# Kernel tuning notes

Measured on AMD Instinct MI355X. Metric: run time of the kernel, lower is better.

## Reference

```python
import jax, jax.numpy as jnp
import numpy as np

EPS = 1e-6
GROUPS = 32


def setup_inputs() -> dict:
    key = jax.random.key(0)
    ks = jax.random.split(key, 6)
    B, C, T = 4, 256, 4096
    s = 1.0 / np.sqrt(C)
    return {
        "x": jax.random.normal(ks[0], (B, C, T), dtype=jnp.float32),
        "gn_scale": jnp.ones((C,), jnp.float32),
        "gn_bias": jnp.zeros((C,), jnp.float32),
        "wq": jax.random.normal(ks[1], (C, C), jnp.float32) * s,
        "bq": jnp.zeros((C,), jnp.float32),
        "wk": jax.random.normal(ks[2], (C, C), jnp.float32) * s,
        "bk": jnp.zeros((C,), jnp.float32),
        "wv": jax.random.normal(ks[3], (C, C), jnp.float32) * s,
        "bv": jnp.zeros((C,), jnp.float32),
        "wo": jax.random.normal(ks[4], (C, C), jnp.float32) * s,
        "bo": jnp.zeros((C,), jnp.float32),
    }


def _group_norm(x, scale, bias):
    B, C, T = x.shape
    h = x.reshape(B, GROUPS, C // GROUPS, T)
    mean = h.mean(axis=(2, 3), keepdims=True)
    var = ((h - mean) ** 2).mean(axis=(2, 3), keepdims=True)
    h = (h - mean) * jax.lax.rsqrt(var + EPS)
    h = h.reshape(B, C, T)
    return h * scale[None, :, None] + bias[None, :, None]


def _conv1x1(w, b, h):
    # Conv1d kernel_size=1 == per-timestep channel matmul
    return jnp.einsum('oc,bct->bot', w, h) + b[None, :, None]


def reference(x, gn_scale, gn_bias, wq, bq, wk, bk, wv, bv, wo, bo):
    B, C, T = x.shape
    h = _group_norm(x, gn_scale, gn_bias)
    q = _conv1x1(wq, bq, h)  # [B,C,T]
    k = _conv1x1(wk, bk, h)
    v = _conv1x1(wv, bv, h)
    # w_[b,q,k] = sum_c q[b,c,q] k[b,c,k] * C**-0.5, softmax over k
    w = jnp.einsum('bcq,bck->bqk', q, k) * (C ** -0.5)
    w = jax.nn.softmax(w, axis=2)
    # torch code: h_[b, i, c] = sum_j w[b, j, i] * v_perm[b, j, c]
    h = jnp.einsum('bqk,bcq->bck', w, v)  # [B,C,T]
    h = _conv1x1(wo, bo, h)
    return x + h
```

## Files before the change

### kernel.cpp

```cpp
#include <hip/hip_runtime.h>

typedef float f32x4 __attribute__((ext_vector_type(4)));
typedef short s16x8 __attribute__((ext_vector_type(8)));

#define MOFF 12.0f

__device__ __forceinline__ unsigned short f2bf(float f) {
  unsigned int u = __float_as_uint(f);
  u += 0x7fffu + ((u >> 16) & 1u);
  return (unsigned short)(u >> 16);
}

template <typename T>
__device__ __forceinline__ void gload16(const T* g, T* l) {
  __builtin_amdgcn_global_load_lds(
      (const __attribute__((address_space(1))) void*)g,
      (__attribute__((address_space(3))) void*)l, 16, 0, 0);
}

__global__ __launch_bounds__(256) void gn_stats_k(const float* __restrict__ x,
                                                  float* __restrict__ meanv,
                                                  float* __restrict__ rstdv) {
  const int bg = blockIdx.x;
  const float4* base = (const float4*)(x + (size_t)bg * 8 * 4096);
  float s = 0.f, q = 0.f;
  for (int i = threadIdx.x; i < 8192; i += 256) {
    float4 v = base[i];
    s += v.x + v.y + v.z + v.w;
    q += v.x * v.x + v.y * v.y + v.z * v.z + v.w * v.w;
  }
  for (int o = 32; o; o >>= 1) { s += __shfl_down(s, o); q += __shfl_down(q, o); }
  __shared__ float ss[4], sq[4];
  const int wv = threadIdx.x >> 6;
  if ((threadIdx.x & 63) == 0) { ss[wv] = s; sq[wv] = q; }
  __syncthreads();
  if (threadIdx.x == 0) {
    s = ss[0] + ss[1] + ss[2] + ss[3];
    q = sq[0] + sq[1] + sq[2] + sq[3];
    float mu = s * (1.f / 32768.f);
    float var = q * (1.f / 32768.f) - mu * mu;
    meanv[bg] = mu;
    rstdv[bg] = rsqrtf(var + 1e-6f);
  }
}

__global__ __launch_bounds__(256) void gn_apply_t_k(const float* __restrict__ x,
    const float* __restrict__ gamma, const float* __restrict__ beta,
    const float* __restrict__ meanv, const float* __restrict__ rstdv,
    unsigned short* __restrict__ hT) {
  __shared__ unsigned short tile[64][72];
  const int b = blockIdx.z, c0 = blockIdx.y * 64, t0 = blockIdx.x * 64;
  const int tid = threadIdx.x;
  {
    const int tr = tid >> 4, tc = (tid & 15) * 4;
    const float* xb = x + ((size_t)b * 256 + c0) * 4096 + t0;
    for (int p2 = 0; p2 < 4; ++p2) {
      int cl = p2 * 16 + tr;
      int c = c0 + cl;
      int bg = b * 32 + (c >> 3);
      float ga = gamma[c] * rstdv[bg];
      float be = beta[c] - meanv[bg] * ga;
      float4 v = *(const float4*)(xb + (size_t)cl * 4096 + tc);
      tile[cl][tc + 0] = f2bf(v.x * ga + be);
      tile[cl][tc + 1] = f2bf(v.y * ga + be);
      tile[cl][tc + 2] = f2bf(v.z * ga + be);
      tile[cl][tc + 3] = f2bf(v.w * ga + be);
    }
  }
  __syncthreads();
  {
    const int orow = tid >> 3, oc = (tid & 7) * 8;
    unsigned short* hb = hT + ((size_t)b * 4096 + t0) * 256 + c0;
    for (int p2 = 0; p2 < 2; ++p2) {
      int tl = p2 * 32 + orow;
      s16x8 w;
#pragma unroll
      for (int j = 0; j < 8; ++j) w[j] = (short)tile[oc + j][tl];
      *(s16x8*)(hb + (size_t)tl * 256 + oc) = w;
    }
  }
}

enum { EPI_WT = 0, EPI_PB = 1, EPI_FIN = 3 };

template <bool AF32, int EPI>
__global__ __launch_bounds__(256) void gemm64_k(
    const void* __restrict__ Ap, long long sA, int lda,
    const unsigned short* __restrict__ Bp, long long sB, int ldb,
    void* __restrict__ Op, long long sO, int ldo,
    const float* __restrict__ bias,
    const float* __restrict__ xadd, long long sX,
    float scale, int K) {
  __shared__ s16x8 lsA[4][64];
  __shared__ s16x8 lsB[4][64];
  const int tid = threadIdx.x;
  const int m0 = blockIdx.y * 64, n0 = blockIdx.x * 64;
  const int z = blockIdx.z;
  const int lane = tid & 63, wv = tid >> 6;
  const int lrow = lane & 15, lg = lane >> 4;
  const int srow = tid >> 2, scg = tid & 3;
  const int swrow = srow ^ (scg << 1);

  f32x4 acc[4];
#pragma unroll
  for (int i = 0; i < 4; ++i) acc[i] = (f32x4){0.f, 0.f, 0.f, 0.f};

  const unsigned short* Bb = Bp + (size_t)z * sB + (size_t)(n0 + srow) * ldb + scg * 8;

  for (int k0 = 0; k0 < K; k0 += 32) {
    if (AF32) {
      const float* ap = (const float*)Ap + (size_t)z * sA + (size_t)(m0 + srow) * lda + k0 + scg * 8;
      float4 v0 = *(const float4*)ap;
      float4 v1 = *(const float4*)(ap + 4);
      s16x8 w;
      w[0] = (short)f2bf(v0.x); w[1] = (short)f2bf(v0.y);
      w[2] = (short)f2bf(v0.z); w[3] = (short)f2bf(v0.w);
      w[4] = (short)f2bf(v1.x); w[5] = (short)f2bf(v1.y);
      w[6] = (short)f2bf(v1.z); w[7] = (short)f2bf(v1.w);
      lsA[scg][swrow] = w;
    } else {
      const unsigned short* ap = (const unsigned short*)Ap + (size_t)z * sA + (size_t)(m0 + srow) * lda + k0 + scg * 8;
      lsA[scg][swrow] = *(const s16x8*)ap;
    }
    lsB[scg][swrow] = *(const s16x8*)(Bb + k0);
    __syncthreads();
    s16x8 af = lsA[lg][(wv * 16 + lrow) ^ (lg << 1)];
#pragma unroll
    for (int nt = 0; nt < 4; ++nt) {
      s16x8 bf = lsB[lg][(nt * 16 + lrow) ^ (lg << 1)];
      acc[nt] = __builtin_amdgcn_mfma_f32_16x16x32_bf16(af, bf, acc[nt], 0, 0, 0);
    }
    __syncthreads();
  }

  const int mb = m0 + wv * 16 + lg * 4;
  float bv0 = 0.f, bv1 = 0.f, bv2 = 0.f, bv3 = 0.f;
  if (bias) { bv0 = bias[mb]; bv1 = bias[mb + 1]; bv2 = bias[mb + 2]; bv3 = bias[mb + 3]; }
#pragma unroll
  for (int nt = 0; nt < 4; ++nt) {
    const int n = n0 + nt * 16 + lrow;
    if (EPI == EPI_WT) {
      ushort4 pk;
      pk.x = f2bf((acc[nt][0] + bv0) * scale);
      pk.y = f2bf((acc[nt][1] + bv1) * scale);
      pk.z = f2bf((acc[nt][2] + bv2) * scale);
      pk.w = f2bf((acc[nt][3] + bv3) * scale);
      *(ushort4*)((unsigned short*)Op + (size_t)z * sO + (size_t)n * ldo + mb) = pk;
    } else if (EPI == EPI_PB) {
      unsigned short* o = (unsigned short*)Op + (size_t)z * sO;
      o[(size_t)(mb + 0) * ldo + n] = f2bf(acc[nt][0] + bv0);
      o[(size_t)(mb + 1) * ldo + n] = f2bf(acc[nt][1] + bv1);
      o[(size_t)(mb + 2) * ldo + n] = f2bf(acc[nt][2] + bv2);
      o[(size_t)(mb + 3) * ldo + n] = f2bf(acc[nt][3] + bv3);
    } else {
      float* o = (float*)Op + (size_t)z * sO;
      const float* xa = xadd + (size_t)z * sX;
      o[(size_t)(mb + 0) * ldo + n] = acc[nt][0] + bv0 + xa[(size_t)(mb + 0) * ldo + n];
      o[(size_t)(mb + 1) * ldo + n] = acc[nt][1] + bv1 + xa[(size_t)(mb + 1) * ldo + n];
      o[(size_t)(mb + 2) * ldo + n] = acc[nt][2] + bv2 + xa[(size_t)(mb + 2) * ldo + n];
      o[(size_t)(mb + 3) * ldo + n] = acc[nt][3] + bv3 + xa[(size_t)(mb + 3) * ldo + n];
    }
  }
}

__global__ __launch_bounds__(256) void attn_stats3_k(
    const unsigned short* __restrict__ qT,
    const unsigned short* __restrict__ kT,
    float* __restrict__ pl) {
  __shared__ unsigned short kbuf[2][64 * 256];
  const int tid = threadIdx.x;
  const int b = blockIdx.z;
  const int Q0 = blockIdx.x * 256;
  const int kc = blockIdx.y;
  const int lane = tid & 63, wq = tid >> 6;
  const int lrow = lane & 15, lg = lane >> 4;

  const unsigned short* qb = qT + (size_t)b * (4096 * 256);
  const unsigned short* kb = kT + (size_t)b * (4096 * 256);

  s16x8 af[4][8];
#pragma unroll
  for (int mt = 0; mt < 4; ++mt)
#pragma unroll
    for (int ks = 0; ks < 8; ++ks)
      af[mt][ks] = *(const s16x8*)(qb + (size_t)(Q0 + wq * 64 + mt * 16 + lrow) * 256 + ks * 32 + lg * 8);

  float sl[4][4];
#pragma unroll
  for (int mt = 0; mt < 4; ++mt)
#pragma unroll
    for (int j = 0; j < 4; ++j) sl[mt][j] = 0.f;

  int cur = 0;
  {
    const unsigned short* src = kb + (size_t)(kc * 512) * 256;
#pragma unroll
    for (int rep = 0; rep < 8; ++rep) {
      int i = rep * 256 + tid;
      int row = i >> 5, c8 = i & 31;
      gload16(src + (size_t)row * 256 + (c8 ^ (row & 7)) * 8, &kbuf[0][(i - lane) * 8]);
    }
  }
  __syncthreads();

  for (int it = 0; it < 8; ++it) {
    if (it + 1 < 8) {
      const unsigned short* src = kb + (size_t)(kc * 512 + (it + 1) * 64) * 256;
#pragma unroll
      for (int rep = 0; rep < 8; ++rep) {
        int i = rep * 256 + tid;
        int row = i >> 5, c8 = i & 31;
        gload16(src + (size_t)row * 256 + (c8 ^ (row & 7)) * 8, &kbuf[cur ^ 1][(i - lane) * 8]);
      }
    }
#pragma unroll
    for (int nt = 0; nt < 4; ++nt) {
      f32x4 acc[4];
#pragma unroll
      for (int mt = 0; mt < 4; ++mt) acc[mt] = (f32x4){0.f, 0.f, 0.f, 0.f};
#pragma unroll
      for (int ks = 0; ks < 8; ++ks) {
        int row = nt * 16 + lrow;
        int ch = (ks * 4 + lg) ^ (row & 7);
        s16x8 bf = *(const s16x8*)&kbuf[cur][row * 256 + ch * 8];
#pragma unroll
        for (int mt = 0; mt < 4; ++mt)
          acc[mt] = __builtin_amdgcn_mfma_f32_16x16x32_bf16(af[mt][ks], bf, acc[mt], 0, 0, 0);
      }
#pragma unroll
      for (int mt = 0; mt < 4; ++mt)
#pragma unroll
        for (int j = 0; j < 4; ++j) sl[mt][j] += __expf(acc[mt][j] - MOFF);
    }
    __syncthreads();
    cur ^= 1;
  }
#pragma unroll
  for (int mt = 0; mt < 4; ++mt)
#pragma unroll
    for (int j = 0; j < 4; ++j) {
      float v = sl[mt][j];
      v += __shfl_xor(v, 1);
      v += __shfl_xor(v, 2);
      v += __shfl_xor(v, 4);
      v += __shfl_xor(v, 8);
      sl[mt][j] = v;
    }
  if (lrow == 0) {
    float* plb = pl + ((size_t)kc * 4 + b) * 4096;
#pragma unroll
    for (int mt = 0; mt < 4; ++mt)
#pragma unroll
      for (int j = 0; j < 4; ++j)
        plb[Q0 + wq * 64 + mt * 16 + lg * 4 + j] = sl[mt][j];
  }
}

__global__ __launch_bounds__(256) void make_r_k(const float* __restrict__ pl,
                                                float* __restrict__ ra) {
  int i = blockIdx.x * 256 + threadIdx.x;
  int b = i >> 12, q = i & 4095;
  float l = 0.f;
#pragma unroll
  for (int kc = 0; kc < 8; ++kc) l += pl[((size_t)kc * 4 + b) * 4096 + q];
  ra[i] = 1.f / l;
}

__global__ __launch_bounds__(512) void attn_pv5_k(
    const unsigned short* __restrict__ qT,
    const unsigned short* __restrict__ kT,
    const unsigned short* __restrict__ vb,
    const float* __restrict__ ra,
    unsigned short* __restrict__ aT) {
  __shared__ unsigned short qbuf[2][128 * 256];
  __shared__ unsigned short P[64 * 128];
  const int tid = threadIdx.x;
  const int pidx = blockIdx.x;
  const int z = (pidx >> 1) & 3;
  const int kt = ((pidx >> 3) << 1) | (pidx & 1);
  const int K0 = kt * 64;
  const int lane = tid & 63, w = tid >> 6;
  const int lrow = lane & 15, lg = lane >> 4;
  const int khw = w >> 2;
  const int qqw = w & 3;

  const unsigned short* qg = qT + (size_t)z * (4096 * 256);
  const unsigned short* kg = kT + (size_t)z * (4096 * 256);
  const unsigned short* vg = vb + (size_t)z * (4096 * 256);
  const float* rg = ra + (size_t)z * 4096;

  s16x8 kf[2][8];
#pragma unroll
  for (int ktl = 0; ktl < 2; ++ktl)
#pragma unroll
    for (int ks = 0; ks < 8; ++ks)
      kf[ktl][ks] = *(const s16x8*)(kg + (size_t)(K0 + khw * 32 + ktl * 16 + lrow) * 256 + ks * 32 + lg * 8);

  f32x4 oacc[2][4];
#pragma unroll
  for (int ct = 0; ct < 2; ++ct)
#pragma unroll
    for (int nt = 0; nt < 4; ++nt) oacc[ct][nt] = (f32x4){0.f, 0.f, 0.f, 0.f};

  int cur = 0;
  {
#pragma unroll
    for (int rep = 0; rep < 8; ++rep) {
      int i = rep * 512 + tid;
      int row = i >> 5, c8 = i & 31;
      gload16(qg + (size_t)row * 256 + (c8 ^ (row & 7)) * 8, &qbuf[0][(i - lane) * 8]);
    }
  }
  __syncthreads();

  for (int qi = 0; qi < 32; ++qi) {
    const int q0 = qi * 128;
    s16x8 vf[2][4];
#pragma unroll
    for (int ct = 0; ct < 2; ++ct)
#pragma unroll
      for (int qs = 0; qs < 4; ++qs)
        vf[ct][qs] = *(const s16x8*)(vg + (size_t)(w * 32 + ct * 16 + lrow) * 4096 + q0 + qs * 32 + lg * 8);
    if (qi + 1 < 32) {
      const unsigned short* src = qg + (size_t)(q0 + 128) * 256;
#pragma unroll
      for (int rep = 0; rep < 8; ++rep) {
        int i = rep * 512 + tid;
        int row = i >> 5, c8 = i & 31;
        gload16(src + (size_t)row * 256 + (c8 ^ (row & 7)) * 8, &qbuf[cur ^ 1][(i - lane) * 8]);
      }
    }
    f32x4 sacc[2][2];
#pragma unroll
    for (int ktl = 0; ktl < 2; ++ktl)
#pragma unroll
      for (int qt = 0; qt < 2; ++qt) sacc[ktl][qt] = (f32x4){0.f, 0.f, 0.f, 0.f};
#pragma unroll
    for (int qt = 0; qt < 2; ++qt) {
#pragma unroll
      for (int ks = 0; ks < 8; ++ks) {
        int row = qqw * 32 + qt * 16 + lrow;
        int ch = (ks * 4 + lg) ^ (row & 7);
        s16x8 qf = *(const s16x8*)&qbuf[cur][row * 256 + ch * 8];
        sacc[0][qt] = __builtin_amdgcn_mfma_f32_16x16x32_bf16(kf[0][ks], qf, sacc[0][qt], 0, 0, 0);
        sacc[1][qt] = __builtin_amdgcn_mfma_f32_16x16x32_bf16(kf[1][ks], qf, sacc[1][qt], 0, 0, 0);
      }
    }
#pragma unroll
    for (int qt = 0; qt < 2; ++qt) {
      const int ql = qqw * 32 + qt * 16 + lrow;
      const float rv = rg[q0 + ql];
#pragma unroll
      for (int ktl = 0; ktl < 2; ++ktl)
#pragma unroll
        for (int j = 0; j < 4; ++j) {
          int k = khw * 32 + ktl * 16 + lg * 4 + j;
          float p = __expf(sacc[ktl][qt][j] - MOFF) * rv;
          P[k * 128 + (((ql >> 3) ^ (k & 7)) << 3) + (ql & 7)] = f2bf(p);
        }
    }
    __syncthreads();
#pragma unroll
    for (int qs = 0; qs < 4; ++qs) {
      s16x8 pf[4];
#pragma unroll
      for (int nt = 0; nt < 4; ++nt) {
        int k = nt * 16 + lrow;
        pf[nt] = *(const s16x8*)&P[k * 128 + (((qs * 4 + lg) ^ (k & 7)) << 3)];
      }
#pragma unroll
      for (int ct = 0; ct < 2; ++ct)
#pragma unroll
        for (int nt = 0; nt < 4; ++nt)
          oacc[ct][nt] = __builtin_amdgcn_mfma_f32_16x16x32_bf16(vf[ct][qs], pf[nt], oacc[ct][nt], 0, 0, 0);
    }
    __syncthreads();
    cur ^= 1;
  }
  unsigned short* ab = aT + (size_t)z * (4096 * 256);
#pragma unroll
  for (int ct = 0; ct < 2; ++ct)
#pragma unroll
    for (int nt = 0; nt < 4; ++nt) {
      int k = K0 + nt * 16 + lrow;
      int c = w * 32 + ct * 16 + lg * 4;
      ushort4 pk;
      pk.x = f2bf(oacc[ct][nt][0]);
      pk.y = f2bf(oacc[ct][nt][1]);
      pk.z = f2bf(oacc[ct][nt][2]);
      pk.w = f2bf(oacc[ct][nt][3]);
      *(ushort4*)(ab + (size_t)k * 256 + c) = pk;
    }
}

extern "C" void kernel_launch(void* const* d_in, const int* in_sizes, int n_in,
                              void* d_out, int out_size, void* d_ws, size_t ws_size,
                              hipStream_t stream) {
  const float* x   = (const float*)d_in[0];
  const float* gns = (const float*)d_in[1];
  const float* gnb = (const float*)d_in[2];
  const float* wq  = (const float*)d_in[3];
  const float* bq  = (const float*)d_in[4];
  const float* wk  = (const float*)d_in[5];
  const float* bk  = (const float*)d_in[6];
  const float* wvp = (const float*)d_in[7];
  const float* bv  = (const float*)d_in[8];
  const float* wo  = (const float*)d_in[9];
  const float* bo  = (const float*)d_in[10];
  float* out = (float*)d_out;

  const int B = 4, C = 256, T = 4096;
  const long long TCe = (long long)T * C;

  char* p = (char*)d_ws;
  unsigned short* hT = (unsigned short*)p; p += (size_t)B * TCe * 2;
  unsigned short* qT = (unsigned short*)p; p += (size_t)B * TCe * 2;
  unsigned short* kT = (unsigned short*)p; p += (size_t)B * TCe * 2;
  unsigned short* vb = (unsigned short*)p; p += (size_t)B * TCe * 2;
  unsigned short* aT = (unsigned short*)p; p += (size_t)B * TCe * 2;
  float* gmean = (float*)p; p += 512;
  float* grstd = (float*)p; p += 512;
  float* pl = (float*)p; p += (size_t)8 * B * T * 4;
  float* ra = (float*)p; p += (size_t)B * T * 4;

  gn_stats_k<<<B * 32, 256, 0, stream>>>(x, gmean, grstd);
  gn_apply_t_k<<<dim3(T / 64, C / 64, B), 256, 0, stream>>>(x, gns, gnb, gmean, grstd, hT);

  gemm64_k<true, EPI_WT><<<dim3(T / 64, C / 64, B), 256, 0, stream>>>(
      wq, 0, C, hT, TCe, C, qT, TCe, C, bq, nullptr, 0, 0.0625f, C);
  gemm64_k<true, EPI_WT><<<dim3(T / 64, C / 64, B), 256, 0, stream>>>(
      wk, 0, C, hT, TCe, C, kT, TCe, C, bk, nullptr, 0, 1.0f, C);
  gemm64_k<true, EPI_PB><<<dim3(T / 64, C / 64, B), 256, 0, stream>>>(
      wvp, 0, C, hT, TCe, C, vb, TCe, T, bv, nullptr, 0, 1.0f, C);

  attn_stats3_k<<<dim3(T / 256, 8, B), 256, 0, stream>>>(qT, kT, pl);
  make_r_k<<<B * T / 256, 256, 0, stream>>>(pl, ra);
  attn_pv5_k<<<256, 512, 0, stream>>>(qT, kT, vb, ra, aT);

  gemm64_k<true, EPI_FIN><<<dim3(T / 64, C / 64, B), 256, 0, stream>>>(
      wo, 0, C, aT, TCe, C, out, TCe, T, bo, x, TCe, 1.0f, C);
}
```

Measured before the change: 206.9 us.

## Split PV attention over query ranges, fold softmax reciprocal into V projection

Reworks the attention PV kernel so each block handles a 128-key tile and one quarter of the queries, with 256-thread blocks, per-wave private P tiles and a smaller Q double buffer. The per-query softmax normalization (1/l) is moved into the V-projection epilogue, which removes the per-element multiply in the hot loop. Partial outputs go to a large fp32 workspace and a new merge kernel sums the four query splits and converts to bf16. The intent is more parallelism and occupancy with less block-level sync, at the cost of extra memory traffic for the fp32 partials and one more launch.

```diff
diff --git a/kernel.cpp b/kernel.cpp
--- a/kernel.cpp
+++ b/kernel.cpp
@@ -81,7 +81,7 @@
   }
 }
 
-enum { EPI_WT = 0, EPI_PB = 1, EPI_FIN = 3 };
+enum { EPI_WT = 0, EPI_PB = 1, EPI_FIN = 3, EPI_PBR = 4 };
 
 template <bool AF32, int EPI>
 __global__ __launch_bounds__(256) void gemm64_k(
@@ -152,6 +152,13 @@
       o[(size_t)(mb + 1) * ldo + n] = f2bf(acc[nt][1] + bv1);
       o[(size_t)(mb + 2) * ldo + n] = f2bf(acc[nt][2] + bv2);
       o[(size_t)(mb + 3) * ldo + n] = f2bf(acc[nt][3] + bv3);
+    } else if (EPI == EPI_PBR) {
+      unsigned short* o = (unsigned short*)Op + (size_t)z * sO;
+      const float rc = (xadd + (size_t)z * sX)[n];
+      o[(size_t)(mb + 0) * ldo + n] = f2bf((acc[nt][0] + bv0) * rc);
+      o[(size_t)(mb + 1) * ldo + n] = f2bf((acc[nt][1] + bv1) * rc);
+      o[(size_t)(mb + 2) * ldo + n] = f2bf((acc[nt][2] + bv2) * rc);
+      o[(size_t)(mb + 3) * ldo + n] = f2bf((acc[nt][3] + bv3) * rc);
     } else {
       float* o = (float*)Op + (size_t)z * sO;
       const float* xa = xadd + (size_t)z * sX;
@@ -266,131 +273,146 @@
   ra[i] = 1.f / l;
 }
 
-__global__ __launch_bounds__(512) void attn_pv5_k(
+__global__ __launch_bounds__(256, 2) void attn_pv17_k(
     const unsigned short* __restrict__ qT,
     const unsigned short* __restrict__ kT,
-    const unsigned short* __restrict__ vb,
-    const float* __restrict__ ra,
-    unsigned short* __restrict__ aT) {
-  __shared__ unsigned short qbuf[2][128 * 256];
-  __shared__ unsigned short P[64 * 128];
+    const unsigned short* __restrict__ vt,
+    float* __restrict__ po) {
+  __shared__ unsigned short qbuf[2][32 * 256];
+  __shared__ unsigned short P[4][32 * 32];
   const int tid = threadIdx.x;
   const int pidx = blockIdx.x;
-  const int z = (pidx >> 1) & 3;
-  const int kt = ((pidx >> 3) << 1) | (pidx & 1);
-  const int K0 = kt * 64;
+  const int a = pidx & 1, z = (pidx >> 1) & 3;
+  const int idx = ((pidx >> 3) << 1) | a;
+  const int ktb = idx & 31, qr = idx >> 5;
   const int lane = tid & 63, w = tid >> 6;
   const int lrow = lane & 15, lg = lane >> 4;
-  const int khw = w >> 2;
-  const int qqw = w & 3;
+  const int K0 = ktb * 128 + w * 32;
+  const int Q0 = qr * 1024;
+  const int lr3 = lrow & 3;
 
   const unsigned short* qg = qT + (size_t)z * (4096 * 256);
   const unsigned short* kg = kT + (size_t)z * (4096 * 256);
-  const unsigned short* vg = vb + (size_t)z * (4096 * 256);
-  const float* rg = ra + (size_t)z * 4096;
+  const unsigned short* vg = vt + (size_t)z * (4096 * 256);
+  unsigned short* Pw = &P[w][0];
 
   s16x8 kf[2][8];
 #pragma unroll
-  for (int ktl = 0; ktl < 2; ++ktl)
+  for (int kt = 0; kt < 2; ++kt)
 #pragma unroll
     for (int ks = 0; ks < 8; ++ks)
-      kf[ktl][ks] = *(const s16x8*)(kg + (size_t)(K0 + khw * 32 + ktl * 16 + lrow) * 256 + ks * 32 + lg * 8);
-
-  f32x4 oacc[2][4];
-#pragma unroll
-  for (int ct = 0; ct < 2; ++ct)
-#pragma unroll
-    for (int nt = 0; nt < 4; ++nt) oacc[ct][nt] = (f32x4){0.f, 0.f, 0.f, 0.f};
+      kf[kt][ks] = *(const s16x8*)(kg + (size_t)(K0 + kt * 16 + lrow) * 256 + ks * 32 + lg * 8);
+
+  f32x4 oacc[16][2];
+#pragma unroll
+  for (int ct = 0; ct < 16; ++ct)
+#pragma unroll
+    for (int kt = 0; kt < 2; ++kt) oacc[ct][kt] = (f32x4){0.f, 0.f, 0.f, 0.f};
 
   int cur = 0;
   {
 #pragma unroll
-    for (int rep = 0; rep < 8; ++rep) {
-      int i = rep * 512 + tid;
+    for (int rep = 0; rep < 4; ++rep) {
+      int i = rep * 256 + tid;
       int row = i >> 5, c8 = i & 31;
-      gload16(qg + (size_t)row * 256 + (c8 ^ (row & 7)) * 8, &qbuf[0][(i - lane) * 8]);
+      gload16(qg + (size_t)(Q0 + row) * 256 + (c8 ^ (row & 7)) * 8, &qbuf[0][(i - lane) * 8]);
     }
   }
   __syncthreads();
 
   for (int qi = 0; qi < 32; ++qi) {
-    const int q0 = qi * 128;
-    s16x8 vf[2][4];
-#pragma unroll
-    for (int ct = 0; ct < 2; ++ct)
-#pragma unroll
-      for (int qs = 0; qs < 4; ++qs)
-        vf[ct][qs] = *(const s16x8*)(vg + (size_t)(w * 32 + ct * 16 + lrow) * 4096 + q0 + qs * 32 + lg * 8);
-    if (qi + 1 < 32) {
-      const unsigned short* src = qg + (size_t)(q0 + 128) * 256;
-#pragma unroll
-      for (int rep = 0; rep < 8; ++rep) {
-        int i = rep * 512 + tid;
+    const int q0 = Q0 + qi * 32;
+    {
+      const int qn = Q0 + ((qi + 1) & 31) * 32;
+#pragma unroll
+      for (int rep = 0; rep < 4; ++rep) {
+        int i = rep * 256 + tid;
         int row = i >> 5, c8 = i & 31;
-        gload16(src + (size_t)row * 256 + (c8 ^ (row & 7)) * 8, &qbuf[cur ^ 1][(i - lane) * 8]);
+        gload16(qg + (size_t)(qn + row) * 256 + (c8 ^ (row & 7)) * 8, &qbuf[cur ^ 1][(i - lane) * 8]);
       }
     }
     f32x4 sacc[2][2];
 #pragma unroll
-    for (int ktl = 0; ktl < 2; ++ktl)
-#pragma unroll
-      for (int qt = 0; qt < 2; ++qt) sacc[ktl][qt] = (f32x4){0.f, 0.f, 0.f, 0.f};
+    for (int kt = 0; kt < 2; ++kt)
+#pragma unroll
+      for (int qt = 0; qt < 2; ++qt) sacc[kt][qt] = (f32x4){0.f, 0.f, 0.f, 0.f};
 #pragma unroll
     for (int qt = 0; qt < 2; ++qt) {
 #pragma unroll
       for (int ks = 0; ks < 8; ++ks) {
-        int row = qqw * 32 + qt * 16 + lrow;
-        int ch = (ks * 4 + lg) ^ (row & 7);
+        const int row = qt * 16 + lrow;
+        const int ch = (ks * 4 + lg) ^ (row & 7);
         s16x8 qf = *(const s16x8*)&qbuf[cur][row * 256 + ch * 8];
-        sacc[0][qt] = __builtin_amdgcn_mfma_f32_16x16x32_bf16(kf[0][ks], qf, sacc[0][qt], 0, 0, 0);
-        sacc[1][qt] = __builtin_amdgcn_mfma_f32_16x16x32_bf16(kf[1][ks], qf, sacc[1][qt], 0, 0, 0);
-      }
-    }
-#pragma unroll
-    for (int qt = 0; qt < 2; ++qt) {
-      const int ql = qqw * 32 + qt * 16 + lrow;
-      const float rv = rg[q0 + ql];
-#pragma unroll
-      for (int ktl = 0; ktl < 2; ++ktl)
-#pragma unroll
-        for (int j = 0; j < 4; ++j) {
-          int k = khw * 32 + ktl * 16 + lg * 4 + j;
-          float p = __expf(sacc[ktl][qt][j] - MOFF) * rv;
-          P[k * 128 + (((ql >> 3) ^ (k & 7)) << 3) + (ql & 7)] = f2bf(p);
-        }
-    }
-    __syncthreads();
-#pragma unroll
-    for (int qs = 0; qs < 4; ++qs) {
-      s16x8 pf[4];
-#pragma unroll
-      for (int nt = 0; nt < 4; ++nt) {
-        int k = nt * 16 + lrow;
-        pf[nt] = *(const s16x8*)&P[k * 128 + (((qs * 4 + lg) ^ (k & 7)) << 3)];
-      }
-#pragma unroll
-      for (int ct = 0; ct < 2; ++ct)
-#pragma unroll
-        for (int nt = 0; nt < 4; ++nt)
-          oacc[ct][nt] = __builtin_amdgcn_mfma_f32_16x16x32_bf16(vf[ct][qs], pf[nt], oacc[ct][nt], 0, 0, 0);
+        sacc[0][qt] = __builtin_amdgcn_mfma_f32_16x16x32_bf16(qf, kf[0][ks], sacc[0][qt], 0, 0, 0);
+        sacc[1][qt] = __builtin_amdgcn_mfma_f32_16x16x32_bf16(qf, kf[1][ks], sacc[1][qt], 0, 0, 0);
+      }
+    }
+#pragma unroll
+    for (int kt = 0; kt < 2; ++kt)
+#pragma unroll
+      for (int qt = 0; qt < 2; ++qt) {
+        const int ql = qt * 16 + lg * 4;
+        const int c0 = (ql >> 3) ^ lr3;
+        ushort4 pk;
+        pk.x = f2bf(__expf(sacc[kt][qt][0] - MOFF));
+        pk.y = f2bf(__expf(sacc[kt][qt][1] - MOFF));
+        pk.z = f2bf(__expf(sacc[kt][qt][2] - MOFF));
+        pk.w = f2bf(__expf(sacc[kt][qt][3] - MOFF));
+        *(ushort4*)&Pw[(kt * 16 + lrow) * 32 + (c0 << 3) + (ql & 7)] = pk;
+      }
+    asm volatile("s_waitcnt lgkmcnt(0)" ::: "memory");
+    __builtin_amdgcn_sched_barrier(0);
+    {
+      s16x8 pf[2];
+#pragma unroll
+      for (int kt = 0; kt < 2; ++kt)
+        pf[kt] = *(const s16x8*)&Pw[(kt * 16 + lrow) * 32 + ((lg ^ lr3) << 3)];
+#pragma unroll
+      for (int h2 = 0; h2 < 2; ++h2) {
+        s16x8 vf[8];
+#pragma unroll
+        for (int i8 = 0; i8 < 8; ++i8)
+          vf[i8] = *(const s16x8*)(vg + (size_t)((h2 * 8 + i8) * 16 + lrow) * 4096 + q0 + lg * 8);
+#pragma unroll
+        for (int i8 = 0; i8 < 8; ++i8)
+#pragma unroll
+          for (int kt = 0; kt < 2; ++kt)
+            oacc[h2 * 8 + i8][kt] = __builtin_amdgcn_mfma_f32_16x16x32_bf16(
+                vf[i8], pf[kt], oacc[h2 * 8 + i8][kt], 0, 0, 0);
+      }
     }
     __syncthreads();
     cur ^= 1;
   }
-  unsigned short* ab = aT + (size_t)z * (4096 * 256);
-#pragma unroll
-  for (int ct = 0; ct < 2; ++ct)
-#pragma unroll
-    for (int nt = 0; nt < 4; ++nt) {
-      int k = K0 + nt * 16 + lrow;
-      int c = w * 32 + ct * 16 + lg * 4;
-      ushort4 pk;
-      pk.x = f2bf(oacc[ct][nt][0]);
-      pk.y = f2bf(oacc[ct][nt][1]);
-      pk.z = f2bf(oacc[ct][nt][2]);
-      pk.w = f2bf(oacc[ct][nt][3]);
-      *(ushort4*)(ab + (size_t)k * 256 + c) = pk;
-    }
+  float* pb = po + (((size_t)(z * 4 + qr)) * 4096) * 256;
+#pragma unroll
+  for (int ct = 0; ct < 16; ++ct)
+#pragma unroll
+    for (int kt = 0; kt < 2; ++kt) {
+      const int k = K0 + kt * 16 + lrow;
+      const int c = ct * 16 + lg * 4;
+      *(float4*)(pb + (size_t)k * 256 + c) = (float4){oacc[ct][kt][0], oacc[ct][kt][1],
+                                                      oacc[ct][kt][2], oacc[ct][kt][3]};
+    }
+}
+
+__global__ __launch_bounds__(256) void merge_k(const float* __restrict__ po,
+                                               unsigned short* __restrict__ aT) {
+  const size_t i = (size_t)blockIdx.x * 256 + threadIdx.x;
+  const size_t n4 = (size_t)4096 * 64;
+  const int b = (int)(i / n4);
+  const size_t r = i - (size_t)b * n4;
+  const float4* p = (const float4*)(po + ((size_t)b * 4) * 4096 * 256) + r;
+  const size_t st = (size_t)4096 * 64;
+  float4 s0 = p[0], s1 = p[st], s2 = p[2 * st], s3 = p[3 * st];
+  float4 s;
+  s.x = s0.x + s1.x + s2.x + s3.x;
+  s.y = s0.y + s1.y + s2.y + s3.y;
+  s.z = s0.z + s1.z + s2.z + s3.z;
+  s.w = s0.w + s1.w + s2.w + s3.w;
+  ushort4 o;
+  o.x = f2bf(s.x); o.y = f2bf(s.y); o.z = f2bf(s.z); o.w = f2bf(s.w);
+  *(ushort4*)(aT + (size_t)b * 4096 * 256 + r * 4) = o;
 }
 
 extern "C" void kernel_launch(void* const* d_in, const int* in_sizes, int n_in,
@@ -422,6 +444,7 @@
   float* grstd = (float*)p; p += 512;
   float* pl = (float*)p; p += (size_t)8 * B * T * 4;
   float* ra = (float*)p; p += (size_t)B * T * 4;
+  float* po = (float*)p; p += (size_t)B * 4 * TCe * 4;
 
   gn_stats_k<<<B * 32, 256, 0, stream>>>(x, gmean, grstd);
   gn_apply_t_k<<<dim3(T / 64, C / 64, B), 256, 0, stream>>>(x, gns, gnb, gmean, grstd, hT);
@@ -430,12 +453,14 @@
       wq, 0, C, hT, TCe, C, qT, TCe, C, bq, nullptr, 0, 0.0625f, C);
   gemm64_k<true, EPI_WT><<<dim3(T / 64, C / 64, B), 256, 0, stream>>>(
       wk, 0, C, hT, TCe, C, kT, TCe, C, bk, nullptr, 0, 1.0f, C);
-  gemm64_k<true, EPI_PB><<<dim3(T / 64, C / 64, B), 256, 0, stream>>>(
-      wvp, 0, C, hT, TCe, C, vb, TCe, T, bv, nullptr, 0, 1.0f, C);
 
   attn_stats3_k<<<dim3(T / 256, 8, B), 256, 0, stream>>>(qT, kT, pl);
   make_r_k<<<B * T / 256, 256, 0, stream>>>(pl, ra);
-  attn_pv5_k<<<256, 512, 0, stream>>>(qT, kT, vb, ra, aT);
+  gemm64_k<true, EPI_PBR><<<dim3(T / 64, C / 64, B), 256, 0, stream>>>(
+      wvp, 0, C, hT, TCe, C, vb, TCe, T, bv, ra, T, 1.0f, C);
+
+  attn_pv17_k<<<512, 256, 0, stream>>>(qT, kT, vb, po);
+  merge_k<<<(int)((size_t)B * TCe / 4 / 256), 256, 0, stream>>>(po, aT);
 
   gemm64_k<true, EPI_FIN><<<dim3(T / 64, C / 64, B), 256, 0, stream>>>(
       wo, 0, C, aT, TCe, C, out, TCe, T, bo, x, TCe, 1.0f, C);
```

Result: slower. 249.7 us (+20.7%).
